# Kernel tuning notes

Hardware: AMD Instinct MI355X
Metric: run time of the kernel (lower is better)

The kernel has to match this reference:

```python
import jax, jax.numpy as jnp
import numpy as np

XSIZE = 128
B = 8
N = 262144


def setup_inputs() -> dict:
    key = jax.random.key(0)
    k1, k2 = jax.random.split(key)
    indices = jax.random.randint(k1, (B, N, 3), 0, XSIZE, dtype=jnp.int32)
    values = jax.random.normal(k2, (B, N), dtype=jnp.float32)
    return {"indices": indices, "values": values, "xsize": XSIZE}


def reference(indices, values, xsize):
    # Batched equivalent of tf.map_fn(tensor_scatter_nd_add) per sample:
    # scatter-add N point values into a zero (xsize, xsize, xsize) grid.
    def build_grid(idx, val):
        grid = jnp.zeros((xsize, xsize, xsize), dtype=val.dtype)
        return grid.at[idx[:, 0], idx[:, 1], idx[:, 2]].add(val)

    grid = jax.vmap(build_grid)(indices, values)  # [B, X, X, X]

    # Adjacent-voxel differences along each spatial axis
    d1 = grid[:, 1:, :, :] - grid[:, :-1, :, :]
    d2 = grid[:, :, 1:, :] - grid[:, :, :-1, :]
    d3 = grid[:, :, :, 1:] - grid[:, :, :, :-1]

    ax = (1, 2, 3)
    # Total variation loss: sum |diff| / num_voxels (xsize^3)
    num_voxels = jnp.float32(xsize * xsize * xsize)
    tv = (jnp.sum(jnp.abs(d1), axis=ax)
          + jnp.sum(jnp.abs(d2), axis=ax)
          + jnp.sum(jnp.abs(d3), axis=ax)) / num_voxels

    # MSE smoothness loss: sum diff^2 / (2*xsize^2 - 2*xsize)
    # (faithful to TF code, which uses only shape[1:3] for the denominator)
    num_pairs = jnp.float32(2 * xsize * xsize - 2 * xsize)
    mse = (jnp.sum(jnp.square(d1), axis=ax)
           + jnp.sum(jnp.square(d2), axis=ax)
           + jnp.sum(jnp.square(d3), axis=ax)) / num_pairs

    return tv, mse
```

## Files before the change

kernel.cpp:

```cpp
#include <hip/hip_runtime.h>

constexpr unsigned XS        = 128;
constexpr unsigned NB        = 8;
constexpr unsigned NPTS      = 262144;
constexpr unsigned TOTAL_PTS = NB * NPTS;
constexpr unsigned PPB       = 4096;
constexpr unsigned NSEG      = TOTAL_PTS / PPB;
constexpr unsigned NBKT      = NB * XS;
constexpr unsigned CAP       = 3072;

constexpr size_t REC2_U64 = (size_t)NBKT * CAP;

__global__ __launch_bounds__(256) void bin_kernel(
        const int* __restrict__ idx, const float* __restrict__ vals,
        unsigned long long* __restrict__ rec2, unsigned* __restrict__ gcur) {
    __shared__ unsigned long long sbuf[PPB];
    __shared__ unsigned hist[XS], cur[XS], loff[XS], gbase[XS];
    unsigned tid = threadIdx.x, g = blockIdx.x;
    unsigned b = g >> 6;
    unsigned base = g * PPB;

    if (tid < XS) hist[tid] = 0u;

    unsigned key[16]; float val[16];
    const unsigned* ibuf = (const unsigned*)sbuf;
    for (unsigned r = 0; r < 4u; ++r) {
        __syncthreads();
        {
            const uint4* src = (const uint4*)idx + ((size_t)g * 3072u + r * 768u);
            uint4* dst = (uint4*)sbuf;
#pragma unroll
            for (unsigned n = 0; n < 3u; ++n) dst[n * 256u + tid] = src[n * 256u + tid];
        }
        __syncthreads();
#pragma unroll
        for (unsigned n = 0; n < 4u; ++n) {
            unsigned p = n * 256u + tid;
            unsigned i = ibuf[3u * p], j = ibuf[3u * p + 1u], k = ibuf[3u * p + 2u];
            unsigned m = r * 4u + n;
            key[m] = (i << 14) | (j << 7) | k;
            val[m] = vals[base + r * 1024u + p];
            atomicAdd(&hist[i], 1u);
        }
    }
    __syncthreads();

    if (tid < 64u) {
        unsigned h0 = hist[tid], h1 = hist[64u + tid];
        unsigned a0 = h0, a1 = h1;
#pragma unroll
        for (unsigned o = 1; o <= 32; o <<= 1) {
            unsigned t0 = __shfl_up(a0, o, 64);
            unsigned t1 = __shfl_up(a1, o, 64);
            if (tid >= o) { a0 += t0; a1 += t1; }
        }
        a1 += __shfl(a0, 63, 64);
        unsigned e0 = a0 - h0, e1 = a1 - h1;
        loff[tid] = e0; loff[64u + tid] = e1;
        cur[tid]  = e0; cur[64u + tid]  = e1;
    }
    __syncthreads();
    if (tid < XS) gbase[tid] = atomicAdd(&gcur[b * XS + tid], hist[tid]);

#pragma unroll
    for (unsigned m = 0; m < 16u; ++m) {
        unsigned i = key[m] >> 14;
        unsigned pos = atomicAdd(&cur[i], 1u);
        sbuf[pos] = ((unsigned long long)__float_as_uint(val[m]) << 32)
                  | (unsigned long long)key[m];
    }
    __syncthreads();

#pragma unroll
    for (unsigned m = 0; m < 16u; ++m) {
        unsigned s = m * 256u + tid;
        unsigned long long rr = sbuf[s];
        unsigned bin = ((unsigned)rr >> 14) & 127u;
        unsigned dst = gbase[bin] + (s - loff[bin]);
        if (dst < CAP)
            rec2[(size_t)(b * XS + bin) * CAP + dst] = rr;
    }
}

__global__ __launch_bounds__(512) void accum_kernel(
        const unsigned long long* __restrict__ rec2,
        const unsigned* __restrict__ gcur, float* __restrict__ stage) {
    __shared__ float strip[65u * XS];
    __shared__ float sred[16];
    unsigned z = blockIdx.x;
    unsigned b = z >> 8, i = (z >> 1) & 127u, h = z & 1u;
    unsigned j0 = h << 6;
    bool has_d1 = (i < 127u);
    unsigned tid = threadIdx.x, lane = tid & 63u, w = tid >> 6;

    unsigned cnt0 = min(gcur[b * XS + i], CAP);
    unsigned cnt1 = has_d1 ? min(gcur[b * XS + i + 1u], CAP) : 0u;
    const unsigned long long* bktA = rec2 + (size_t)(b * XS + i) * CAP;
    const unsigned long long* bktB = bktA + CAP;

    unsigned long long rvA[6]; bool avA[6];
#pragma unroll
    for (unsigned q = 0; q < 6u; ++q) {
        unsigned r = q * 512u + tid;
        avA[q] = r < cnt0;
        if (avA[q]) rvA[q] = bktA[r];
    }

    float4* p4 = (float4*)strip;
    for (unsigned r = tid; r < 2080u; r += 512u)
        p4[r] = float4{0.f, 0.f, 0.f, 0.f};
    __syncthreads();

#pragma unroll
    for (unsigned q = 0; q < 6u; ++q)
        if (avA[q]) {
            unsigned kk = (unsigned)rvA[q];
            unsigned j = (kk >> 7) & 127u;
            unsigned l = j - j0;
            if (l <= 64u)
                atomicAdd(&strip[(l << 7) | (kk & 127u)],
                          __uint_as_float((unsigned)(rvA[q] >> 32)));
        }
    __syncthreads();

    unsigned long long rvB[6]; bool avB[6];
    if (has_d1) {
#pragma unroll
        for (unsigned q = 0; q < 6u; ++q) {
            unsigned r = q * 512u + tid;
            avB[q] = r < cnt1;
            if (avB[q]) rvB[q] = bktB[r];
        }
    }

    unsigned jmax = 127u - j0;
    float tv = 0.f, mse = 0.f;
#pragma unroll
    for (unsigned r = 0; r < 4u; ++r) {
        unsigned v4 = r * 512u + tid;
        unsigned l = v4 >> 5, k4 = v4 & 31u;
        float4 c = p4[v4];
        float d0 = c.y - c.x, d1 = c.z - c.y, d2 = c.w - c.z;
        tv  += fabsf(d0) + fabsf(d1) + fabsf(d2);
        mse += d0 * d0 + d1 * d1 + d2 * d2;
        if (k4 < 31u) {
            float nx = strip[(v4 << 2) + 4u];
            float d3 = nx - c.w;
            tv += fabsf(d3); mse += d3 * d3;
        }
        if (l < jmax) {
            float4 n = p4[v4 + 32u];
            float e0 = n.x - c.x, e1 = n.y - c.y, e2 = n.z - c.z, e3 = n.w - c.w;
            tv  += fabsf(e0) + fabsf(e1) + fabsf(e2) + fabsf(e3);
            mse += e0 * e0 + e1 * e1 + e2 * e2 + e3 * e3;
        }
    }

    if (has_d1) {
        __syncthreads();
#pragma unroll
        for (unsigned q = 0; q < 6u; ++q)
            if (avB[q]) {
                unsigned kk = (unsigned)rvB[q];
                unsigned j = (kk >> 7) & 127u;
                unsigned l = j - j0;
                if (l <= 63u)
                    atomicAdd(&strip[(l << 7) | (kk & 127u)],
                              -__uint_as_float((unsigned)(rvB[q] >> 32)));
            }
        __syncthreads();
#pragma unroll
        for (unsigned r = 0; r < 4u; ++r) {
            float4 dd = p4[r * 512u + tid];
            tv  += fabsf(dd.x) + fabsf(dd.y) + fabsf(dd.z) + fabsf(dd.w);
            mse += dd.x * dd.x + dd.y * dd.y + dd.z * dd.z + dd.w * dd.w;
        }
    }

#pragma unroll
    for (int o = 32; o > 0; o >>= 1) {
        tv  += __shfl_down(tv, o, 64);
        mse += __shfl_down(mse, o, 64);
    }
    if (lane == 0u) { sred[w] = tv; sred[8u + w] = mse; }
    __syncthreads();
    if (tid == 0u) {
        float tt = 0.f, mm = 0.f;
#pragma unroll
        for (unsigned q = 0; q < 8u; ++q) { tt += sred[q]; mm += sred[8u + q]; }
        atomicAdd(stage + (size_t)b * 16u,        tt);
        atomicAdd(stage + (size_t)(8u + b) * 16u, mm);
    }
}

__global__ void finalize_kernel(const float* __restrict__ stage,
                                float* __restrict__ out) {
    unsigned i = threadIdx.x;
    if (i < 16u) {
        float s = stage[i * 16u];
        float scale = (i < 8u) ? (1.0f / 2097152.0f)
                               : (1.0f / 32512.0f);
        out[i] = s * scale;
    }
}

extern "C" void kernel_launch(void* const* d_in, const int* in_sizes, int n_in,
                              void* d_out, int out_size, void* d_ws, size_t ws_size,
                              hipStream_t stream) {
    const int*   idx  = (const int*)d_in[0];
    const float* vals = (const float*)d_in[1];

    unsigned long long* rec2 = (unsigned long long*)d_ws;
    unsigned* gcur  = (unsigned*)(rec2 + REC2_U64);
    float*    stage = (float*)(gcur + NBKT);
    float*    out   = (float*)d_out;

    hipMemsetAsync(gcur, 0, NBKT * 4 + 256 * 4, stream);

    bin_kernel<<<NSEG, 256, 0, stream>>>(idx, vals, rec2, gcur);
    accum_kernel<<<2u * NBKT, 512, 0, stream>>>(rec2, gcur, stage);
    finalize_kernel<<<1, 64, 0, stream>>>(stage, out);
}
```

Baseline: 115.7 us.

## Bin points by (i, j-half) so accum blocks read only their own half

Binning now uses 256 buckets per sample, keyed by i and the half of j, and duplicates j==64 points into the lower-half bucket as its halo row. Each accum block reads only its own bucket of about 1k records instead of the full i-slab of about 2k, which removes half the record loads and the per-record j filtering. Records are pre-encoded with their local strip offset, so the shared-memory atomics need only a mask. The costs are more histogram atomics, a variable-length scatter loop in the bin kernel, and a smaller per-bucket capacity of 1536, which narrows overflow headroom.

After: 118.0 us. +2.1%, slower.

```diff
diff --git a/kernel.cpp b/kernel.cpp
--- a/kernel.cpp
+++ b/kernel.cpp
@@ -6,21 +6,25 @@
 constexpr unsigned TOTAL_PTS = NB * NPTS;
 constexpr unsigned PPB       = 4096;
 constexpr unsigned NSEG      = TOTAL_PTS / PPB;
-constexpr unsigned NBKT      = NB * XS;
-constexpr unsigned CAP       = 3072;
+constexpr unsigned NBIN      = 256;
+constexpr unsigned NBKT      = NB * NBIN;
+constexpr unsigned CAP       = 1536;
+constexpr unsigned STGCAP    = PPB + 256;
 
 constexpr size_t REC2_U64 = (size_t)NBKT * CAP;
+
 
 __global__ __launch_bounds__(256) void bin_kernel(
         const int* __restrict__ idx, const float* __restrict__ vals,
         unsigned long long* __restrict__ rec2, unsigned* __restrict__ gcur) {
-    __shared__ unsigned long long sbuf[PPB];
-    __shared__ unsigned hist[XS], cur[XS], loff[XS], gbase[XS];
+    __shared__ unsigned long long sbuf[STGCAP];
+    __shared__ unsigned hist[NBIN], cur[NBIN], loff[NBIN], gbase[NBIN];
+    __shared__ unsigned sntot;
     unsigned tid = threadIdx.x, g = blockIdx.x;
     unsigned b = g >> 6;
     unsigned base = g * PPB;
 
-    if (tid < XS) hist[tid] = 0u;
+    hist[tid] = 0u;
 
     unsigned key[16]; float val[16];
     const unsigned* ibuf = (const unsigned*)sbuf;
@@ -40,45 +44,59 @@
             unsigned m = r * 4u + n;
             key[m] = (i << 14) | (j << 7) | k;
             val[m] = vals[base + r * 1024u + p];
-            atomicAdd(&hist[i], 1u);
+            atomicAdd(&hist[(i << 1) | (j >> 6)], 1u);
+            if (j == 64u) atomicAdd(&hist[i << 1], 1u);
         }
     }
     __syncthreads();
 
     if (tid < 64u) {
-        unsigned h0 = hist[tid], h1 = hist[64u + tid];
-        unsigned a0 = h0, a1 = h1;
-#pragma unroll
-        for (unsigned o = 1; o <= 32; o <<= 1) {
-            unsigned t0 = __shfl_up(a0, o, 64);
-            unsigned t1 = __shfl_up(a1, o, 64);
-            if (tid >= o) { a0 += t0; a1 += t1; }
-        }
-        a1 += __shfl(a0, 63, 64);
-        unsigned e0 = a0 - h0, e1 = a1 - h1;
-        loff[tid] = e0; loff[64u + tid] = e1;
-        cur[tid]  = e0; cur[64u + tid]  = e1;
-    }
-    __syncthreads();
-    if (tid < XS) gbase[tid] = atomicAdd(&gcur[b * XS + tid], hist[tid]);
+        unsigned carry = 0u;
+#pragma unroll
+        for (unsigned c = 0; c < 4u; ++c) {
+            unsigned hh = hist[c * 64u + tid];
+            unsigned a = hh;
+#pragma unroll
+            for (unsigned o = 1; o <= 32; o <<= 1) {
+                unsigned t = __shfl_up(a, o, 64);
+                if (tid >= o) a += t;
+            }
+            unsigned e = a - hh + carry;
+            loff[c * 64u + tid] = e;
+            cur[c * 64u + tid]  = e;
+            carry += __shfl(a, 63, 64);
+        }
+        if (tid == 0u) sntot = carry;
+    }
+    __syncthreads();
+
+    gbase[tid] = atomicAdd(&gcur[b * NBIN + tid], hist[tid]);
 
 #pragma unroll
     for (unsigned m = 0; m < 16u; ++m) {
-        unsigned i = key[m] >> 14;
-        unsigned pos = atomicAdd(&cur[i], 1u);
-        sbuf[pos] = ((unsigned long long)__float_as_uint(val[m]) << 32)
-                  | (unsigned long long)key[m];
-    }
-    __syncthreads();
-
-#pragma unroll
-    for (unsigned m = 0; m < 16u; ++m) {
-        unsigned s = m * 256u + tid;
+        unsigned kk = key[m];
+        unsigned i = kk >> 14, j = (kk >> 7) & 127u, k = kk & 127u;
+        unsigned be = (i << 1) | (j >> 6);
+        unsigned long long vb = (unsigned long long)__float_as_uint(val[m]) << 32;
+        unsigned pos = atomicAdd(&cur[be], 1u);
+        if (pos < STGCAP)
+            sbuf[pos] = vb | (be << 14) | ((j & 63u) << 7) | k;
+        if (j == 64u) {
+            unsigned be2 = i << 1;
+            unsigned pos2 = atomicAdd(&cur[be2], 1u);
+            if (pos2 < STGCAP)
+                sbuf[pos2] = vb | (be2 << 14) | (64u << 7) | k;
+        }
+    }
+    __syncthreads();
+
+    unsigned ntot = sntot;
+    for (unsigned s = tid; s < ntot; s += 256u) {
         unsigned long long rr = sbuf[s];
-        unsigned bin = ((unsigned)rr >> 14) & 127u;
-        unsigned dst = gbase[bin] + (s - loff[bin]);
+        unsigned be = ((unsigned)rr >> 14) & 0xFFu;
+        unsigned dst = gbase[be] + (s - loff[be]);
         if (dst < CAP)
-            rec2[(size_t)(b * XS + bin) * CAP + dst] = rr;
+            rec2[(size_t)(b * NBIN + be) * CAP + dst] = rr;
     }
 }
 
@@ -88,19 +106,20 @@
     __shared__ float strip[65u * XS];
     __shared__ float sred[16];
     unsigned z = blockIdx.x;
-    unsigned b = z >> 8, i = (z >> 1) & 127u, h = z & 1u;
+    unsigned b = z >> 8, rem = z & 255u;
+    unsigned i = rem >> 1, h = rem & 1u;
     unsigned j0 = h << 6;
     bool has_d1 = (i < 127u);
     unsigned tid = threadIdx.x, lane = tid & 63u, w = tid >> 6;
 
-    unsigned cnt0 = min(gcur[b * XS + i], CAP);
-    unsigned cnt1 = has_d1 ? min(gcur[b * XS + i + 1u], CAP) : 0u;
-    const unsigned long long* bktA = rec2 + (size_t)(b * XS + i) * CAP;
-    const unsigned long long* bktB = bktA + CAP;
-
-    unsigned long long rvA[6]; bool avA[6];
-#pragma unroll
-    for (unsigned q = 0; q < 6u; ++q) {
+    unsigned cnt0 = min(gcur[b * NBIN + rem], CAP);
+    unsigned cnt1 = has_d1 ? min(gcur[b * NBIN + rem + 2u], CAP) : 0u;
+    const unsigned long long* bktA = rec2 + (size_t)(b * NBIN + rem) * CAP;
+    const unsigned long long* bktB = bktA + 2u * (size_t)CAP;
+
+    unsigned long long rvA[3]; bool avA[3];
+#pragma unroll
+    for (unsigned q = 0; q < 3u; ++q) {
         unsigned r = q * 512u + tid;
         avA[q] = r < cnt0;
         if (avA[q]) rvA[q] = bktA[r];
@@ -112,21 +131,16 @@
     __syncthreads();
 
 #pragma unroll
-    for (unsigned q = 0; q < 6u; ++q)
-        if (avA[q]) {
-            unsigned kk = (unsigned)rvA[q];
-            unsigned j = (kk >> 7) & 127u;
-            unsigned l = j - j0;
-            if (l <= 64u)
-                atomicAdd(&strip[(l << 7) | (kk & 127u)],
-                          __uint_as_float((unsigned)(rvA[q] >> 32)));
-        }
-    __syncthreads();
-
-    unsigned long long rvB[6]; bool avB[6];
+    for (unsigned q = 0; q < 3u; ++q)
+        if (avA[q])
+            atomicAdd(&strip[(unsigned)rvA[q] & 0x3FFFu],
+                      __uint_as_float((unsigned)(rvA[q] >> 32)));
+    __syncthreads();
+
+    unsigned long long rvB[3]; bool avB[3];
     if (has_d1) {
 #pragma unroll
-        for (unsigned q = 0; q < 6u; ++q) {
+        for (unsigned q = 0; q < 3u; ++q) {
             unsigned r = q * 512u + tid;
             avB[q] = r < cnt1;
             if (avB[q]) rvB[q] = bktB[r];
@@ -159,13 +173,11 @@
     if (has_d1) {
         __syncthreads();
 #pragma unroll
-        for (unsigned q = 0; q < 6u; ++q)
+        for (unsigned q = 0; q < 3u; ++q)
             if (avB[q]) {
-                unsigned kk = (unsigned)rvB[q];
-                unsigned j = (kk >> 7) & 127u;
-                unsigned l = j - j0;
-                if (l <= 63u)
-                    atomicAdd(&strip[(l << 7) | (kk & 127u)],
+                unsigned a = (unsigned)rvB[q] & 0x3FFFu;
+                if (a < 8192u)
+                    atomicAdd(&strip[a],
                               -__uint_as_float((unsigned)(rvB[q] >> 32)));
             }
         __syncthreads();
@@ -218,6 +230,6 @@
     hipMemsetAsync(gcur, 0, NBKT * 4 + 256 * 4, stream);
 
     bin_kernel<<<NSEG, 256, 0, stream>>>(idx, vals, rec2, gcur);
-    accum_kernel<<<2u * NBKT, 512, 0, stream>>>(rec2, gcur, stage);
+    accum_kernel<<<NB * NBIN, 512, 0, stream>>>(rec2, gcur, stage);
     finalize_kernel<<<1, 64, 0, stream>>>(stage, out);
 }
```
